# Performance work log

Measured on AMD Instinct MI355X. Metric: run time of the kernel, lower is better.

## Reference

```python
import jax, jax.numpy as jnp
import numpy as np

BIG = 1e6  # sentinel 'no zero pixel found yet' distance; BIG**2 = 1e12 fits fp32


def _edt(is_fg):
    """Exact Euclidean distance transform (scipy.distance_transform_edt semantics):
    distance from each nonzero pixel to the nearest zero pixel. is_fg: [N,H,W] bool.
    Separable exact algorithm: 1D vertical distance-to-zero per column via cummax
    scans, then min-plus convolution with the parabola (j-k)^2 along rows."""
    N, H, W = is_fg.shape
    is_zero = ~is_fg
    ih = jnp.arange(H, dtype=jnp.float32)[None, :, None]
    # nearest zero at-or-above / at-or-below along H (per column)
    up = jax.lax.cummax(jnp.where(is_zero, ih, -BIG), axis=1)
    dn = -jax.lax.cummax(jnp.where(is_zero, -ih, -BIG), axis=1, reverse=True)
    g = jnp.minimum(ih - up, dn - ih)               # [N,H,W] vertical 1D distance
    g2 = jnp.minimum(g, BIG) ** 2
    ks = jnp.arange(W, dtype=jnp.float32)
    def col(j):
        # exact 2D squared distance for output column j: min_k (j-k)^2 + g(.,.,k)^2
        return jnp.min((j.astype(jnp.float32) - ks) ** 2 + g2, axis=-1)  # [N,H]
    d2 = jax.lax.map(col, jnp.arange(W))            # [W,N,H], sequential -> low memory
    return jnp.sqrt(jnp.moveaxis(d2, 0, -1))        # [N,H,W]


def setup_inputs() -> dict:
    key = jax.random.key(0)
    k1, k2 = jax.random.split(key)
    B, C, H, W = 8, 12, 256, 256
    logits = jax.random.normal(k1, (B, C, H, W), dtype=jnp.float32)
    targets = jax.random.randint(k2, (B, H, W), 0, C, dtype=jnp.int32)
    return {"logits": logits, "targets": targets}


def reference(logits, targets):
    B, C, H, W = logits.shape
    probs = jax.nn.softmax(logits, axis=1)                                  # [B,C,H,W]
    gt = targets[:, None, :, :] == jnp.arange(C, dtype=targets.dtype)[None, :, None, None]
    m = gt.reshape(B * C, H, W)
    pos = _edt(m)          # distance inside foreground to nearest background
    neg = _edt(~m)         # distance inside background to nearest foreground
    dt = (neg - pos).reshape(B, C, H, W)
    has_fg = gt.any(axis=(2, 3))                                            # [B,C]
    dt = jnp.where(has_fg[:, :, None, None], dt, 0.0)
    # per-image, per-class min-max normalization (matches torch view(B,-1).min/max)
    dmin = dt.min(axis=(2, 3), keepdims=True)
    dmax = dt.max(axis=(2, 3), keepdims=True)
    dt = (dt - dmin) / (dmax - dmin + 1e-8)
    inter = jnp.sum(probs * dt, axis=(2, 3))                                # [B,C]
    denom = jnp.sum(probs * probs, axis=(2, 3)) + jnp.sum(dt * dt, axis=(2, 3)) + 1e-6
    dice = 2.0 * inter / denom
    # sum_c mean_b (1-dice) / C  == mean over (b,c) since ignore_index=255 is out of range
    return jnp.mean(1.0 - dice)
```

## Files before the change

kernel.cpp:

```cpp
#include <hip/hip_runtime.h>
#include <math.h>

constexpr int B_  = 8;
constexpr int C_  = 12;
constexpr int H_  = 256;
constexpr int W_  = 256;
constexpr int HW_ = H_ * W_;
constexpr int NBC_ = B_ * C_;
constexpr int PAD_ = 256;
constexpr int VB_  = NBC_ * 8;


__global__ void k_vp(const int* __restrict__ t,
                     const float* __restrict__ logits,
                     unsigned short* __restrict__ gpk,
                     int* __restrict__ hasfg_p,
                     float2* __restrict__ den,
                     float* __restrict__ out) {
    int tid = threadIdx.x;
    if (blockIdx.x >= VB_) {
        int pb = blockIdx.x - VB_;
        int b = pb >> 8;
        int p = ((pb & 255) << 8) + tid;
        const float* lb = logits + (size_t)b * C_ * HW_ + p;
        float l[C_];
        float mxl = -3.4e38f;
        #pragma unroll
        for (int c = 0; c < C_; ++c) { l[c] = lb[c * HW_]; mxl = fmaxf(mxl, l[c]); }
        float s = 0.f;
        #pragma unroll
        for (int c = 0; c < C_; ++c) s += __expf(l[c] - mxl);
        den[(size_t)b * HW_ + p] = make_float2(mxl, 1.0f / s);
        return;
    }

    if (blockIdx.x == 0 && tid == 0) out[0] = 0.0f;
    constexpr int SEG = 8, SH = 32;
    int s  = tid >> 5;
    int wl = tid & 31;
    int blk = blockIdx.x;
    int bc = blk >> 3;
    int w0 = (blk & 7) * 32;
    int b = bc / C_, c = bc - b * C_;
    int w = w0 + wl;
    const int* base = t + b * HW_ + w;
    int h0 = s * SH;

    unsigned tp[SH / 4];
    int lastEq = -1, lastNeq = -1, firstEq = 256, firstNeq = 256;
    #pragma unroll 8
    for (int i = 0; i < SH; ++i) {
        int tv = base[(h0 + i) * W_];
        if ((i & 3) == 0) tp[i >> 2] = 0;
        tp[i >> 2] |= (unsigned)tv << ((i & 3) * 8);
        int h = h0 + i;
        if (tv == c) { lastEq = h;  if (firstEq  == 256) firstEq  = h; }
        else         { lastNeq = h; if (firstNeq == 256) firstNeq = h; }
    }
    __shared__ int sLE[SEG][32], sLN[SEG][32], sFE[SEG][32], sFN[SEG][32];
    sLE[s][wl] = lastEq; sLN[s][wl] = lastNeq;
    sFE[s][wl] = firstEq; sFN[s][wl] = firstNeq;
    __syncthreads();

    int carLE = -1, carLN = -1;
    for (int q = 0; q < s; ++q) {
        carLE = max(carLE, sLE[q][wl]);
        carLN = max(carLN, sLN[q][wl]);
    }
    int carFE = 256, carFN = 256;
    for (int q = s + 1; q < SEG; ++q) {
        carFE = min(carFE, sFE[q][wl]);
        carFN = min(carFN, sFN[q][wl]);
    }
    bool pred = (s == SEG - 1) && (max(carLE, lastEq) >= 0);
    bool anyfg = __any(pred);
    if (tid == 192) hasfg_p[blk] = anyfg ? 1 : 0;

    int pLE[SH], pLN[SH];
    {
        int le = carLE, ln = carLN;
        #pragma unroll
        for (int i = 0; i < SH; ++i) {
            int tv = (tp[i >> 2] >> ((i & 3) * 8)) & 0xFF;
            int h = h0 + i;
            if (tv == c) le = h; else ln = h;
            pLE[i] = le; pLN[i] = ln;
        }
    }
    {
        int fe = carFE, fn = carFN;
        unsigned short* gk = gpk + (size_t)bc * HW_ + w;
        #pragma unroll
        for (int i = SH - 1; i >= 0; --i) {
            int tv = (tp[i >> 2] >> ((i & 3) * 8)) & 0xFF;
            int h = h0 + i;
            if (tv == c) fe = h; else fn = h;
            bool fg = (tv == c);
            int lastZ = fg ? pLN[i] : pLE[i];
            int nextZ = fg ? fn : fe;
            int dl  = (lastZ < 0)   ? 0x7FFF : (h - lastZ);
            int dnx = (nextZ > 255) ? 0x7FFF : (nextZ - h);
            int d = min(dl, dnx);
            gk[h * W_] = (unsigned short)(d | (fg ? 0x8000 : 0));
        }
    }
}

__global__ void k_edt(const unsigned short* __restrict__ gpk,
                      const float* __restrict__ logits,
                      const float2* __restrict__ den,
                      const int* __restrict__ hasfg_p,
                      float* __restrict__ part) {
    __shared__ float sp[4][W_ + 2 * PAD_];
    __shared__ float sn[4][W_ + 2 * PAD_];
    int wave = threadIdx.x >> 6;
    int lane = threadIdx.x & 63;
    int row = blockIdx.x * 4 + wave;
    int bc = row >> 8;
    int b = bc / C_, c = bc - b * C_;
    int h = row & (H_ - 1);

    int hfl = 0;
    if (lane < 8) hfl = hasfg_p[bc * 8 + lane];
    bool hf = __any(hfl != 0);

    float dv[4];
    if (hf) {
        float4 inf4 = make_float4(3.0e38f, 3.0e38f, 3.0e38f, 3.0e38f);
        ((float4*)&sp[wave][0])[lane]          = inf4;
        ((float4*)&sp[wave][PAD_ + W_])[lane]  = inf4;
        ((float4*)&sn[wave][0])[lane]          = inf4;
        ((float4*)&sn[wave][PAD_ + W_])[lane]  = inf4;

        float s1 = (float)(1000000 - h);
        float sent2 = s1 * s1;
        const ushort4 v4 = ((const ushort4*)(gpk + (size_t)row * W_))[lane];
        float4 fpv, fnv;
        {
            const unsigned short* vs = (const unsigned short*)&v4;
            float* fp = (float*)&fpv;
            float* fn = (float*)&fnv;
            #pragma unroll
            for (int q = 0; q < 4; ++q) {
                unsigned v = vs[q];
                unsigned d = v & 0x7FFFu;
                float g2 = (d == 0x7FFFu) ? sent2 : (float)(d * d);
                bool fg = (v & 0x8000u) != 0;
                fp[q] = fg ? g2 : 0.0f;
                fn[q] = fg ? 0.0f : g2;
            }
        }
        ((float4*)&sp[wave][PAD_])[lane] = fpv;
        ((float4*)&sn[wave][PAD_])[lane] = fnv;
        __syncthreads();

        float bp[4], bn[4];
        #pragma unroll
        for (int i = 0; i < 4; ++i) {
            int j = PAD_ + lane + 64 * i;
            bp[i] = sp[wave][j];
            bn[i] = sn[wave][j];
        }
        for (int r = 1; r < W_; ++r) {
            float fr = (float)r;
            float r2 = fr * fr;
            float m = fmaxf(fmaxf(bn[0], bn[1]), fmaxf(bn[2], bn[3]));
            if (!__any(r2 < m)) break;
            #pragma unroll
            for (int i = 0; i < 4; ++i) {
                int j = PAD_ + lane + 64 * i;
                float v = fminf(sn[wave][j - r], sn[wave][j + r]);
                bn[i] = fminf(bn[i], fmaf(fr, fr, v));
            }
        }
        for (int r = 1; r < W_; ++r) {
            float fr = (float)r;
            float r2 = fr * fr;
            float m = fmaxf(fmaxf(bp[0], bp[1]), fmaxf(bp[2], bp[3]));
            if (!__any(r2 < m)) break;
            #pragma unroll
            for (int i = 0; i < 4; ++i) {
                int j = PAD_ + lane + 64 * i;
                float v = fminf(sp[wave][j - r], sp[wave][j + r]);
                bp[i] = fminf(bp[i], fmaf(fr, fr, v));
            }
        }
        #pragma unroll
        for (int i = 0; i < 4; ++i) dv[i] = sqrtf(bn[i]) - sqrtf(bp[i]);
    } else {
        #pragma unroll
        for (int i = 0; i < 4; ++i) dv[i] = 0.0f;
    }

    const float*  lrow = logits + ((size_t)b * C_ + c) * HW_ + h * W_;
    const float2* drow = den + (size_t)b * HW_ + h * W_;
    float s_pd = 0.f, s_p = 0.f, s_pp = 0.f, s_d = 0.f, s_dd = 0.f;
    float mn = 3.4e38f, mx = -3.4e38f;
    #pragma unroll
    for (int i = 0; i < 4; ++i) {
        int j = lane + 64 * i;
        float2 mi = drow[j];
        float pr = __expf(lrow[j] - mi.x) * mi.y;
        float d = dv[i];
        s_pd = fmaf(pr, d, s_pd);
        s_p += pr;
        s_pp = fmaf(pr, pr, s_pp);
        s_d += d;
        s_dd = fmaf(d, d, s_dd);
        mn = fminf(mn, d);
        mx = fmaxf(mx, d);
    }
    #pragma unroll
    for (int off = 32; off; off >>= 1) {
        s_pd += __shfl_down(s_pd, off);
        s_p  += __shfl_down(s_p, off);
        s_pp += __shfl_down(s_pp, off);
        s_d  += __shfl_down(s_d, off);
        s_dd += __shfl_down(s_dd, off);
        mn = fminf(mn, __shfl_down(mn, off));
        mx = fmaxf(mx, __shfl_down(mx, off));
    }
    if (lane == 0) {
        float* p8 = part + (size_t)row * 8;
        p8[0] = s_pd; p8[1] = s_p; p8[2] = s_pp;
        p8[3] = s_d;  p8[4] = s_dd; p8[5] = mn; p8[6] = mx;
    }
}

__global__ void k_bcred(const float* __restrict__ part, float* __restrict__ out) {
    int bc = blockIdx.x;
    int tid = threadIdx.x;
    const float* p8 = part + ((size_t)bc * 256 + tid) * 8;
    float s_pd = p8[0], s_p = p8[1], s_pp = p8[2];
    float s_d = p8[3], s_dd = p8[4], mn = p8[5], mx = p8[6];
    #pragma unroll
    for (int off = 32; off; off >>= 1) {
        s_pd += __shfl_down(s_pd, off);
        s_p  += __shfl_down(s_p, off);
        s_pp += __shfl_down(s_pp, off);
        s_d  += __shfl_down(s_d, off);
        s_dd += __shfl_down(s_dd, off);
        mn = fminf(mn, __shfl_down(mn, off));
        mx = fmaxf(mx, __shfl_down(mx, off));
    }
    __shared__ float red[4][7];
    int wave = tid >> 6, lane = tid & 63;
    if (lane == 0) {
        red[wave][0] = s_pd; red[wave][1] = s_p; red[wave][2] = s_pp;
        red[wave][3] = s_d;  red[wave][4] = s_dd; red[wave][5] = mn; red[wave][6] = mx;
    }
    __syncthreads();
    if (tid == 0) {
        s_pd = red[0][0]; s_p = red[0][1]; s_pp = red[0][2];
        s_d = red[0][3]; s_dd = red[0][4]; mn = red[0][5]; mx = red[0][6];
        for (int w = 1; w < 4; ++w) {
            s_pd += red[w][0]; s_p += red[w][1]; s_pp += red[w][2];
            s_d += red[w][3]; s_dd += red[w][4];
            mn = fminf(mn, red[w][5]); mx = fmaxf(mx, red[w][6]);
        }
        float sc = 1.0f / (mx - mn + 1e-8f);
        float inter = sc * (s_pd - mn * s_p);
        float d2 = sc * sc * (s_dd - 2.0f * mn * s_d + mn * mn * (float)HW_);
        float dice = 2.0f * inter / (s_pp + d2 + 1e-6f);
        atomicAdd(out, (1.0f - dice) * (1.0f / (float)NBC_));
    }
}

extern "C" void kernel_launch(void* const* d_in, const int* in_sizes, int n_in,
                              void* d_out, int out_size, void* d_ws, size_t ws_size,
                              hipStream_t stream) {
    const float* logits  = (const float*)d_in[0];
    const int*   targets = (const int*)d_in[1];
    float* out = (float*)d_out;

    unsigned short* gpk = (unsigned short*)d_ws;
    int* hasfg_p = (int*)(gpk + (size_t)NBC_ * HW_);
    float* part = (float*)(hasfg_p + NBC_ * 8);
    float2* den = (float2*)(part + (size_t)NBC_ * H_ * 8);

    k_vp<<<VB_ + B_ * (HW_ / 256), 256, 0, stream>>>(targets, logits, gpk,
                                                     hasfg_p, den, out);
    k_edt<<<NBC_ * H_ / 4, 256, 0, stream>>>(gpk, logits, den, hasfg_p, part);
    k_bcred<<<NBC_, 256, 0, stream>>>(part, out);
}
```

Before: 105.6 us.

## Shrink EDT shared padding, drop block sync, prefetch logits/den with vector loads

```diff
diff --git a/kernel.cpp b/kernel.cpp
--- a/kernel.cpp
+++ b/kernel.cpp
@@ -7,7 +7,8 @@
 constexpr int W_  = 256;
 constexpr int HW_ = H_ * W_;
 constexpr int NBC_ = B_ * C_;
-constexpr int PAD_ = 256;
+constexpr int PAD_ = 64;
+constexpr int LW_  = W_ + 2 * PAD_;
 constexpr int VB_  = NBC_ * 8;
 
 
@@ -106,13 +107,14 @@
     }
 }
 
-__global__ void k_edt(const unsigned short* __restrict__ gpk,
-                      const float* __restrict__ logits,
-                      const float2* __restrict__ den,
-                      const int* __restrict__ hasfg_p,
-                      float* __restrict__ part) {
-    __shared__ float sp[4][W_ + 2 * PAD_];
-    __shared__ float sn[4][W_ + 2 * PAD_];
+__global__ void __launch_bounds__(256, 8)
+k_edt(const unsigned short* __restrict__ gpk,
+      const float* __restrict__ logits,
+      const float2* __restrict__ den,
+      const int* __restrict__ hasfg_p,
+      float* __restrict__ part) {
+    __shared__ float sp[4][LW_];
+    __shared__ float sn[4][LW_];
     int wave = threadIdx.x >> 6;
     int lane = threadIdx.x & 63;
     int row = blockIdx.x * 4 + wave;
@@ -120,17 +122,25 @@
     int b = bc / C_, c = bc - b * C_;
     int h = row & (H_ - 1);
 
+    const float*  lrow = logits + ((size_t)b * C_ + c) * HW_ + h * W_;
+    const float2* drow = den + (size_t)b * HW_ + h * W_;
+    float4 lv  = ((const float4*)lrow)[lane];
+    float4 dn0 = ((const float4*)drow)[lane * 2];
+    float4 dn1 = ((const float4*)drow)[lane * 2 + 1];
+
     int hfl = 0;
     if (lane < 8) hfl = hasfg_p[bc * 8 + lane];
     bool hf = __any(hfl != 0);
 
-    float dv[4];
+    float4 d4;
     if (hf) {
         float4 inf4 = make_float4(3.0e38f, 3.0e38f, 3.0e38f, 3.0e38f);
-        ((float4*)&sp[wave][0])[lane]          = inf4;
-        ((float4*)&sp[wave][PAD_ + W_])[lane]  = inf4;
-        ((float4*)&sn[wave][0])[lane]          = inf4;
-        ((float4*)&sn[wave][PAD_ + W_])[lane]  = inf4;
+        if (lane < PAD_ / 4) {
+            ((float4*)&sp[wave][0])[lane]         = inf4;
+            ((float4*)&sp[wave][PAD_ + W_])[lane] = inf4;
+            ((float4*)&sn[wave][0])[lane]         = inf4;
+            ((float4*)&sn[wave][PAD_ + W_])[lane] = inf4;
+        }
 
         float s1 = (float)(1000000 - h);
         float sent2 = s1 * s1;
@@ -152,7 +162,6 @@
         }
         ((float4*)&sp[wave][PAD_])[lane] = fpv;
         ((float4*)&sn[wave][PAD_])[lane] = fnv;
-        __syncthreads();
 
         float bp[4], bn[4];
         #pragma unroll
@@ -166,11 +175,21 @@
             float r2 = fr * fr;
             float m = fmaxf(fmaxf(bn[0], bn[1]), fmaxf(bn[2], bn[3]));
             if (!__any(r2 < m)) break;
-            #pragma unroll
-            for (int i = 0; i < 4; ++i) {
-                int j = PAD_ + lane + 64 * i;
-                float v = fminf(sn[wave][j - r], sn[wave][j + r]);
-                bn[i] = fminf(bn[i], fmaf(fr, fr, v));
+            if (r < PAD_) {
+                #pragma unroll
+                for (int i = 0; i < 4; ++i) {
+                    int j = PAD_ + lane + 64 * i;
+                    float v = fminf(sn[wave][j - r], sn[wave][j + r]);
+                    bn[i] = fminf(bn[i], fmaf(fr, fr, v));
+                }
+            } else {
+                #pragma unroll
+                for (int i = 0; i < 4; ++i) {
+                    int j = PAD_ + lane + 64 * i;
+                    float v = fminf(sn[wave][max(j - r, 0)],
+                                    sn[wave][min(j + r, LW_ - 1)]);
+                    bn[i] = fminf(bn[i], fmaf(fr, fr, v));
+                }
             }
         }
         for (int r = 1; r < W_; ++r) {
@@ -178,33 +197,45 @@
             float r2 = fr * fr;
             float m = fmaxf(fmaxf(bp[0], bp[1]), fmaxf(bp[2], bp[3]));
             if (!__any(r2 < m)) break;
-            #pragma unroll
-            for (int i = 0; i < 4; ++i) {
-                int j = PAD_ + lane + 64 * i;
-                float v = fminf(sp[wave][j - r], sp[wave][j + r]);
-                bp[i] = fminf(bp[i], fmaf(fr, fr, v));
+            if (r < PAD_) {
+                #pragma unroll
+                for (int i = 0; i < 4; ++i) {
+                    int j = PAD_ + lane + 64 * i;
+                    float v = fminf(sp[wave][j - r], sp[wave][j + r]);
+                    bp[i] = fminf(bp[i], fmaf(fr, fr, v));
+                }
+            } else {
+                #pragma unroll
+                for (int i = 0; i < 4; ++i) {
+                    int j = PAD_ + lane + 64 * i;
+                    float v = fminf(sp[wave][max(j - r, 0)],
+                                    sp[wave][min(j + r, LW_ - 1)]);
+                    bp[i] = fminf(bp[i], fmaf(fr, fr, v));
+                }
             }
         }
         #pragma unroll
-        for (int i = 0; i < 4; ++i) dv[i] = sqrtf(bn[i]) - sqrtf(bp[i]);
+        for (int i = 0; i < 4; ++i)
+            sn[wave][PAD_ + lane + 64 * i] = sqrtf(bn[i]) - sqrtf(bp[i]);
+        d4 = ((float4*)&sn[wave][PAD_])[lane];
     } else {
-        #pragma unroll
-        for (int i = 0; i < 4; ++i) dv[i] = 0.0f;
-    }
-
-    const float*  lrow = logits + ((size_t)b * C_ + c) * HW_ + h * W_;
-    const float2* drow = den + (size_t)b * HW_ + h * W_;
+        d4 = make_float4(0.f, 0.f, 0.f, 0.f);
+    }
+
+    float pr[4];
+    pr[0] = __expf(lv.x - dn0.x) * dn0.y;
+    pr[1] = __expf(lv.y - dn0.z) * dn0.w;
+    pr[2] = __expf(lv.z - dn1.x) * dn1.y;
+    pr[3] = __expf(lv.w - dn1.z) * dn1.w;
+    const float* dq = (const float*)&d4;
     float s_pd = 0.f, s_p = 0.f, s_pp = 0.f, s_d = 0.f, s_dd = 0.f;
     float mn = 3.4e38f, mx = -3.4e38f;
     #pragma unroll
-    for (int i = 0; i < 4; ++i) {
-        int j = lane + 64 * i;
-        float2 mi = drow[j];
-        float pr = __expf(lrow[j] - mi.x) * mi.y;
-        float d = dv[i];
-        s_pd = fmaf(pr, d, s_pd);
-        s_p += pr;
-        s_pp = fmaf(pr, pr, s_pp);
+    for (int q = 0; q < 4; ++q) {
+        float p = pr[q], d = dq[q];
+        s_pd = fmaf(p, d, s_pd);
+        s_p += p;
+        s_pp = fmaf(p, p, s_pp);
         s_d += d;
         s_dd = fmaf(d, d, s_dd);
         mn = fminf(mn, d);
```

New measurement: 106.7 us. No clear change (+1.0%).
